# Performance work log

Measured on AMD Instinct MI355X. Metric: run time of the kernel, lower is better.

## Reference

```python
import jax, jax.numpy as jnp
import numpy as np
from jax import lax

# ---- constants matching init_kwargs ----
NY, NX = 1024, 1024
DX, DY = 50.0, 50.0
TTOT = 32.0
DTMAX = 0.5
RHO, G, FD = 910.0, 9.81, 1e-17
EPS = 1e-10
T_FREQ = 5.0
N_STEPS = 64            # fixed step count (>= TTOT/DTMAX); dt masked to 0 once time >= TTOT
LAPSE = 0.0065          # degC per m elevation lapse rate (SMB model)
MELT_FACTOR = 0.5       # m ice / (degC * yr) ablation factor (SMB model)


def update_smb(Z_surf, precip, T_ma_lowest, T_mj_lowest, ice_mask):
    # Lapse-rate temperatures at the surface
    T_ma = T_ma_lowest - LAPSE * Z_surf   # mean annual temperature
    T_mj = T_mj_lowest - LAPSE * Z_surf   # mean July temperature
    accumulation = precip * (T_ma < 0.0).astype(Z_surf.dtype)
    ablation = MELT_FACTOR * jnp.maximum(T_mj, 0.0)
    return (accumulation - ablation) * ice_mask


def setup_inputs() -> dict:
    key = jax.random.key(0)
    k1, k2, k3 = jax.random.split(key, 3)
    # smooth mountain topography: 2500 m gaussian massif + small noise
    y = np.arange(NY, dtype=np.float32) * DY
    x = np.arange(NX, dtype=np.float32) * DX
    yy, xx = np.meshgrid(y, x, indexing="ij")
    cy, cx = y.mean(), x.mean()
    sigma = 0.25 * NX * DX
    z = 2500.0 * np.exp(-((yy - cy) ** 2 + (xx - cx) ** 2) / (2.0 * sigma ** 2))
    Z_topo = jnp.asarray(z, dtype=jnp.float32) + 5.0 * jax.random.normal(k1, (NY, NX), dtype=jnp.float32)
    precip_tensor = 2.0 * jax.random.uniform(k2, (NY, NX), dtype=jnp.float32)  # m ice / yr
    T_ma_lowest = jnp.float32(8.0) + jax.random.normal(k3, (), dtype=jnp.float32)
    T_mj_lowest = T_ma_lowest + jnp.float32(8.0)
    ice_mask = jnp.ones((NY, NX), dtype=jnp.float32)
    return {"precip_tensor": precip_tensor, "T_ma_lowest": T_ma_lowest,
            "T_mj_lowest": T_mj_lowest, "Z_topo": Z_topo, "ice_mask": ice_mask}


def _glacier_step(carry, _, Z_topo, precip, T_ma_lowest, T_mj_lowest, ice_mask):
    H_ice, Z_surf, smb, time, t_last = carry
    # staggered-grid averages and slopes (SIA diffusion)
    H_avg = 0.25 * (H_ice[:-1, :-1] + H_ice[1:, 1:] + H_ice[:-1, 1:] + H_ice[1:, :-1])
    Sx = (Z_surf[:, 1:] - Z_surf[:, :-1]) / DX
    Sy = (Z_surf[1:, :] - Z_surf[:-1, :]) / DY
    Sx = 0.5 * (Sx[:-1, :] + Sx[1:, :])          # (NY-1, NX-1)
    Sy = 0.5 * (Sy[:, :-1] + Sy[:, 1:])          # (NY-1, NX-1)
    Snorm = jnp.sqrt(Sx ** 2 + Sy ** 2 + EPS)
    D = FD * (RHO * G) ** 3 * H_avg ** 5 * Snorm ** 2 + EPS
    # adaptive CFL dt; torch uses .item() so dt is a non-differentiable constant
    dt = jnp.minimum(min(DX, DY) ** 2 / (2.7 * jnp.max(D)), DTMAX)
    dt = lax.stop_gradient(dt)
    dt = jnp.where(time < TTOT, dt, 0.0)         # freeze once ttot is reached
    qx = -(0.5 * (D[:-1, :] + D[1:, :])) * (Z_surf[1:-1, 1:] - Z_surf[1:-1, :-1]) / DX
    qy = -(0.5 * (D[:, :-1] + D[:, 1:])) * (Z_surf[1:, 1:-1] - Z_surf[:-1, 1:-1]) / DY
    dHdt = -(jnp.diff(qx, axis=1) / DX + jnp.diff(qy, axis=0) / DY)  # (NY-2, NX-2)
    H_new = H_ice.at[1:-1, 1:-1].add(dt * (dHdt + smb[1:-1, 1:-1]))
    H_new = jnp.maximum(H_new, 0.0)
    Z_new = Z_topo + H_new
    time = time + dt
    # refresh SMB every T_FREQ model years
    do_upd = (time - t_last) >= T_FREQ
    smb_new = update_smb(Z_new, precip, T_ma_lowest, T_mj_lowest, ice_mask)
    smb = jnp.where(do_upd, smb_new, smb)
    t_last = jnp.where(do_upd, time, t_last)
    return (H_new, Z_new, smb, time, t_last), None


def reference(precip_tensor, T_ma_lowest, T_mj_lowest, Z_topo, ice_mask):
    H_ice = jnp.zeros((NY, NX), dtype=jnp.float32)
    Z_surf = Z_topo + H_ice
    smb = update_smb(Z_surf, precip_tensor, T_ma_lowest, T_mj_lowest, ice_mask)
    time = jnp.float32(0.0)
    t_last = jnp.float32(0.0)
    step = lambda c, x: _glacier_step(c, x, Z_topo, precip_tensor, T_ma_lowest, T_mj_lowest, ice_mask)
    (H_ice, _, _, _, _), _ = lax.scan(step, (H_ice, Z_surf, smb, time, t_last), None, length=N_STEPS)
    return H_ice
```

## Files before the change

kernel.cpp:

```cpp
#include <hip/hip_runtime.h>
#include <math.h>

#define NYg 1024
#define NXg 1024
#define W   1024
#define NSTEPS 64
#define GRID_N (NYg * W)
#define NB    256

#define NSLOT 16
#define SLOT_STRIDE 32
#define SLOT_GROUP  (NSLOT * SLOT_STRIDE)
#define NSLOTG      (NSTEPS + 1)
#define WS_CNT  (NSLOTG * SLOT_GROUP)
#define WS_NBF  (WS_CNT + NSLOT * 32)
#define WS_CTRL_END (WS_NBF + NB * 32)
#define WS_GRIDS 65536

constexpr float DXf   = 50.0f;
constexpr float DYf   = 50.0f;
constexpr float TTOTf = 32.0f;
constexpr float DTMAXf= 0.5f;
constexpr float EPSf  = 1e-10f;
constexpr float TFREQ = 5.0f;
constexpr float LAPSE = 0.0065f;
constexpr float MELTF = 0.5f;
constexpr double RHOG = 910.0 * 9.81;
constexpr float  CDf  = (float)(1e-17 * RHOG * RHOG * RHOG);

__device__ __forceinline__ float scloadf(const float* p) {
    return __hip_atomic_load(p, __ATOMIC_RELAXED, __HIP_MEMORY_SCOPE_SYSTEM);
}
__device__ __forceinline__ void scstoref(float* p, float v) {
    __hip_atomic_store(p, v, __ATOMIC_RELAXED, __HIP_MEMORY_SCOPE_SYSTEM);
}
__device__ __forceinline__ unsigned scloadu(const unsigned* p) {
    return __hip_atomic_load(p, __ATOMIC_RELAXED, __HIP_MEMORY_SCOPE_SYSTEM);
}

__device__ __forceinline__ void poll_backoff(int& sp) {
    if (sp < 32) { __builtin_amdgcn_s_sleep(1); ++sp; }
    else           __builtin_amdgcn_s_sleep(8);
}

__device__ __forceinline__ float dfunc(float h00, float h01, float h10, float h11,
                                       float z00, float z01, float z10, float z11)
{
    float havg = 0.25f * (h00 + h11 + h01 + h10);
    float sx = ((z01 - z00) + (z11 - z10)) * (0.5f / DXf);
    float sy = ((z10 - z00) + (z11 - z01)) * (0.5f / DYf);
    float sn = sqrtf(sx * sx + sy * sy + EPSf);
    float h2 = havg * havg;
    float h4 = h2 * h2;
    return CDf * (h4 * havg) * (sn * sn) + EPSf;
}

__global__ __launch_bounds__(256) void k_init(unsigned* __restrict__ ctrl)
{
    int idx = blockIdx.x * blockDim.x + threadIdx.x;
    int stride = gridDim.x * blockDim.x;
    for (int i = idx; i < WS_CTRL_END; i += stride) {
        unsigned v = 0u;
        if (i < SLOT_GROUP && (i & (SLOT_STRIDE - 1)) == 0) v = __float_as_uint(EPSf);
        ctrl[i] = v;
    }
}

__global__ __launch_bounds__(1024, 1) void k_run(
    float* __restrict__ EZ0, float* __restrict__ EZ1,
    float* __restrict__ ED0, float* __restrict__ ED1,
    const float* __restrict__ ztopo, const float* __restrict__ precip,
    const float* __restrict__ mask, const float* __restrict__ tma,
    const float* __restrict__ tmj, unsigned* __restrict__ ctrl,
    float* __restrict__ Hout)
{
    __shared__ float sZ[7][W];
    __shared__ float sHm[5][W];
    __shared__ float sD[6][W];
    __shared__ unsigned su[NSLOT];
    __shared__ float smax16[16];

    unsigned* slots = ctrl;
    unsigned* cnt   = ctrl + WS_CNT;
    unsigned* nbf   = ctrl + WS_NBF;

    const int c   = threadIdx.x;
    const int b   = blockIdx.x;
    const int r0  = b * 4;
    const int grp = b & (NSLOT - 1);
    const int lane = c & 63, wid = c >> 6;
    const bool hasA = (b > 0), hasB = (b < NB - 1);

    const float TMA = tma[0], TMJ = tmj[0];

    float smbr[5], ztr[5], hN[5], zN[5];
    float dh[5], hOld[5], zOld[5];
    bool inter[5];

    auto c1row = [&](int rr) {
        int r = r0 + rr;
        float zc = 0.0f, hc = 0.0f, d = 0.0f;
        bool iv = false;
        if (r < NYg) {
            zc = sZ[rr + 1][c];
            hc = sHm[rr][c];
            iv = (r >= 1 && r <= NYg - 2 && c >= 1 && c <= NXg - 2);
            if (iv) {
                float zl = sZ[rr + 1][c - 1], zr = sZ[rr + 1][c + 1];
                float zt = sZ[rr][c],         zb = sZ[rr + 2][c];
                float d00 = sD[rr][c - 1],     d01 = sD[rr][c];
                float d10 = sD[rr + 1][c - 1], d11 = sD[rr + 1][c];
                float qxR = -0.5f * (d01 + d11) * (zr - zc) * (1.0f / DXf);
                float qxL = -0.5f * (d00 + d10) * (zc - zl) * (1.0f / DXf);
                float qyB = -0.5f * (d10 + d11) * (zb - zc) * (1.0f / DYf);
                float qyT = -0.5f * (d00 + d01) * (zc - zt) * (1.0f / DYf);
                d = -((qxR - qxL) * (1.0f / DXf) + (qyB - qyT) * (1.0f / DYf));
            }
        }
        dh[rr] = d; hOld[rr] = hc; zOld[rr] = zc; inter[rr] = iv;
    };

    #pragma unroll
    for (int q = 0; q < 7; ++q) {
        int r = r0 - 1 + q;
        sZ[q][c] = (r >= 0 && r < NYg) ? ztopo[r * W + c] : 0.0f;
    }
    #pragma unroll
    for (int q = 0; q < 5; ++q) sHm[q][c] = 0.0f;
    #pragma unroll
    for (int q = 0; q < 6; ++q) sD[q][c] = EPSf;
    #pragma unroll
    for (int rr = 0; rr < 5; ++rr) {
        int r = r0 + rr;
        if (r < NYg) {
            float z = ztopo[r * W + c];
            ztr[rr] = z;
            float t_ma = TMA - LAPSE * z;
            float t_mj = TMJ - LAPSE * z;
            float acc  = (t_ma < 0.0f) ? precip[r * W + c] : 0.0f;
            float abl  = MELTF * fmaxf(t_mj, 0.0f);
            smbr[rr] = (acc - abl) * mask[r * W + c];
        } else { ztr[rr] = 0.0f; smbr[rr] = 0.0f; }
    }
    __syncthreads();

    float t = 0.0f, tl = 0.0f;

    for (int s = 0; s < NSTEPS; ++s) {
        const float* EZr = (s & 1) ? EZ1 : EZ0;
        float*       EZw = (s & 1) ? EZ0 : EZ1;
        const float* EDr = (s & 1) ? ED1 : ED0;
        float*       EDw = (s & 1) ? ED0 : ED1;

        if (s > 0) {
            if (c == 0 && hasA) {
                int sp = 0;
                while (scloadu(&nbf[(b - 1) * 32]) < (unsigned)s) poll_backoff(sp);
            }
            if (c == 64 && hasB) {
                int sp = 0;
                while (scloadu(&nbf[(b + 1) * 32]) < (unsigned)s) poll_backoff(sp);
            }
            __syncthreads();
            float zA = 0.0f, zB = 0.0f, dA = 0.0f, dB = 0.0f;
            if (hasA) { zA = scloadf(EZr + (r0 - 1) * W + c);
                        if (c <= NXg - 2) dA = scloadf(EDr + (r0 - 1) * W + c); }
            if (hasB) { zB = scloadf(EZr + (r0 + 5) * W + c);
                        if (c <= NXg - 2) dB = scloadf(EDr + (r0 + 4) * W + c); }
            c1row(1); c1row(2); c1row(3);
            if (hasA) { sZ[0][c] = zA; if (c <= NXg - 2) sD[0][c] = dA; }
            if (hasB) { sZ[6][c] = zB; if (c <= NXg - 2) sD[5][c] = dB; }
            __syncthreads();
            c1row(0); c1row(4);
        } else {
            c1row(0); c1row(1); c1row(2); c1row(3); c1row(4);
        }

        if (c < NSLOT) {
            unsigned tgt = 16u * (unsigned)s;
            int sp = 0;
            while (scloadu(&cnt[c * 32]) < tgt) poll_backoff(sp);
            su[c] = scloadu(&slots[s * SLOT_GROUP + c * SLOT_STRIDE]);
        }
        __syncthreads();

        unsigned mb = su[0];
        #pragma unroll
        for (int q = 1; q < NSLOT; ++q) mb = max(mb, su[q]);
        float mD = __uint_as_float(mb);
        float dt = fminf(2500.0f / (2.7f * mD), DTMAXf);
        if (!(t < TTOTf)) dt = 0.0f;
        float nt  = t + dt;
        bool  upd = (nt - tl) >= TFREQ;

        #pragma unroll
        for (int rr = 0; rr < 5; ++rr) {
            int r = r0 + rr;
            float h, z;
            if (r >= NYg)        { h = 0.0f; z = 0.0f; }
            else if (inter[rr])  { h = fmaxf(hOld[rr] + dt * (dh[rr] + smbr[rr]), 0.0f);
                                   z = ztr[rr] + h; }
            else                 { h = 0.0f; z = zOld[rr]; }
            hN[rr] = h; zN[rr] = z;
            if (r < NYg) { sZ[rr + 1][c] = z; sHm[rr][c] = h; }
        }
        __syncthreads();

        if (s < NSTEPS - 1) {
            float m = 0.0f, d0 = 0.0f, d3 = 0.0f;
            #pragma unroll
            for (int rr = 0; rr < 4; ++rr) {
                int i = r0 + rr;
                if (i <= NYg - 2 && c <= NXg - 2) {
                    float d = dfunc(sHm[rr][c], sHm[rr][c + 1],
                                    sHm[rr + 1][c], sHm[rr + 1][c + 1],
                                    sZ[rr + 1][c], sZ[rr + 1][c + 1],
                                    sZ[rr + 2][c], sZ[rr + 2][c + 1]);
                    sD[rr + 1][c] = d;
                    m = fmaxf(m, d);
                    if (rr == 0) d0 = d;
                    if (rr == 3) d3 = d;
                }
            }
            #pragma unroll
            for (int off = 32; off >= 1; off >>= 1)
                m = fmaxf(m, __shfl_xor(m, off, 64));
            if (lane == 0) smax16[wid] = m;
            __syncthreads();
            if (c == 0) {
                #pragma unroll
                for (int q = 1; q < 16; ++q) m = fmaxf(m, smax16[q]);
                __hip_atomic_fetch_max(&slots[(s + 1) * SLOT_GROUP + grp * SLOT_STRIDE],
                                       __float_as_uint(m),
                                       __ATOMIC_RELAXED, __HIP_MEMORY_SCOPE_SYSTEM);
                asm volatile("s_waitcnt vmcnt(0)" ::: "memory");
                __hip_atomic_fetch_add(&cnt[grp * 32], 1u,
                                       __ATOMIC_RELAXED, __HIP_MEMORY_SCOPE_SYSTEM);
            }
            if (hasA) {
                scstoref(EZw + (r0 + 1) * W + c, zN[1]);
                if (c <= NXg - 2 && r0 <= NYg - 2) scstoref(EDw + r0 * W + c, d0);
            }
            if (hasB) {
                scstoref(EZw + (r0 + 3) * W + c, zN[3]);
                if (c <= NXg - 2 && r0 + 3 <= NYg - 2) scstoref(EDw + (r0 + 3) * W + c, d3);
            }
            asm volatile("s_waitcnt vmcnt(0)" ::: "memory");
            __syncthreads();
            if (c == 0)
                __hip_atomic_store(&nbf[b * 32], (unsigned)(s + 1),
                                   __ATOMIC_RELAXED, __HIP_MEMORY_SCOPE_SYSTEM);

            if (upd) {
                #pragma unroll
                for (int rr = 0; rr < 5; ++rr) {
                    int r = r0 + rr;
                    if (r < NYg) {
                        float z = zN[rr];
                        float t_ma = TMA - LAPSE * z;
                        float t_mj = TMJ - LAPSE * z;
                        float acc  = (t_ma < 0.0f) ? precip[r * W + c] : 0.0f;
                        float abl  = MELTF * fmaxf(t_mj, 0.0f);
                        smbr[rr] = (acc - abl) * mask[r * W + c];
                    }
                }
            }
        }

        t = nt;
        if (upd) tl = nt;
    }

    #pragma unroll
    for (int rr = 0; rr < 4; ++rr)
        Hout[(r0 + rr) * W + c] = hN[rr];
}

extern "C" void kernel_launch(void* const* d_in, const int* in_sizes, int n_in,
                              void* d_out, int out_size, void* d_ws, size_t ws_size,
                              hipStream_t stream)
{
    const float* precip = (const float*)d_in[0];
    const float* tma    = (const float*)d_in[1];
    const float* tmj    = (const float*)d_in[2];
    const float* ztopo  = (const float*)d_in[3];
    const float* mask   = (const float*)d_in[4];

    unsigned* ctrl = (unsigned*)d_ws;
    float* g = (float*)d_ws + WS_GRIDS;
    float* EZ0 = g + 0 * GRID_N;
    float* EZ1 = g + 1 * GRID_N;
    float* ED0 = g + 2 * GRID_N;
    float* ED1 = g + 3 * GRID_N;

    k_init<<<dim3(64), dim3(256), 0, stream>>>(ctrl);

    k_run<<<dim3(NB), dim3(1024), 0, stream>>>(EZ0, EZ1, ED0, ED1,
                                               ztopo, precip, mask, tma, tmj,
                                               ctrl, (float*)d_out);
}
```

Baseline: 466.0 us.

## Replace counter-based global barrier with per-block max slots polled in parallel

Each block now writes its local max diffusivity into its own slot per step (nonzero value doubles as a ready flag), and 256 threads poll all slots in parallel and reduce with shuffles. This replaces the atomic fetch-max and fetch-add counters and the separate neighbor flags. The dt is computed before the flux pass, so the update is fused into the row computation and one barrier and round trip per step are removed. Halo readiness is implied by the slot write that follows the halo stores. Risk: 256 pollers per block add memory traffic, and correctness relies on the slot store being ordered after the halo stores (vmcnt wait plus barrier).

After: 587.9 us. +26.2%, slower.

```diff
diff --git a/kernel.cpp b/kernel.cpp
--- a/kernel.cpp
+++ b/kernel.cpp
@@ -8,13 +8,8 @@
 #define GRID_N (NYg * W)
 #define NB    256
 
-#define NSLOT 16
-#define SLOT_STRIDE 32
-#define SLOT_GROUP  (NSLOT * SLOT_STRIDE)
-#define NSLOTG      (NSTEPS + 1)
-#define WS_CNT  (NSLOTG * SLOT_GROUP)
-#define WS_NBF  (WS_CNT + NSLOT * 32)
-#define WS_CTRL_END (WS_NBF + NB * 32)
+#define NSLOTG (NSTEPS + 1)
+#define WS_CTRL_END (NSLOTG * NB)
 #define WS_GRIDS 65536
 
 constexpr float DXf   = 50.0f;
@@ -37,6 +32,9 @@
 __device__ __forceinline__ unsigned scloadu(const unsigned* p) {
     return __hip_atomic_load(p, __ATOMIC_RELAXED, __HIP_MEMORY_SCOPE_SYSTEM);
 }
+__device__ __forceinline__ void scstoreu(unsigned* p, unsigned v) {
+    __hip_atomic_store(p, v, __ATOMIC_RELAXED, __HIP_MEMORY_SCOPE_SYSTEM);
+}
 
 __device__ __forceinline__ void poll_backoff(int& sp) {
     if (sp < 32) { __builtin_amdgcn_s_sleep(1); ++sp; }
@@ -59,11 +57,8 @@
 {
     int idx = blockIdx.x * blockDim.x + threadIdx.x;
     int stride = gridDim.x * blockDim.x;
-    for (int i = idx; i < WS_CTRL_END; i += stride) {
-        unsigned v = 0u;
-        if (i < SLOT_GROUP && (i & (SLOT_STRIDE - 1)) == 0) v = __float_as_uint(EPSf);
-        ctrl[i] = v;
-    }
+    for (int i = idx; i < WS_CTRL_END; i += stride) ctrl[i] = 0u;
+    if (idx < NB) ctrl[idx] = __float_as_uint(EPSf);
 }
 
 __global__ __launch_bounds__(1024, 1) void k_run(
@@ -71,41 +66,32 @@
     float* __restrict__ ED0, float* __restrict__ ED1,
     const float* __restrict__ ztopo, const float* __restrict__ precip,
     const float* __restrict__ mask, const float* __restrict__ tma,
-    const float* __restrict__ tmj, unsigned* __restrict__ ctrl,
+    const float* __restrict__ tmj, unsigned* __restrict__ slots,
     float* __restrict__ Hout)
 {
     __shared__ float sZ[7][W];
     __shared__ float sHm[5][W];
     __shared__ float sD[6][W];
-    __shared__ unsigned su[NSLOT];
+    __shared__ unsigned su4[4];
     __shared__ float smax16[16];
-
-    unsigned* slots = ctrl;
-    unsigned* cnt   = ctrl + WS_CNT;
-    unsigned* nbf   = ctrl + WS_NBF;
 
     const int c   = threadIdx.x;
     const int b   = blockIdx.x;
     const int r0  = b * 4;
-    const int grp = b & (NSLOT - 1);
     const int lane = c & 63, wid = c >> 6;
     const bool hasA = (b > 0), hasB = (b < NB - 1);
 
     const float TMA = tma[0], TMJ = tmj[0];
 
     float smbr[5], ztr[5], hN[5], zN[5];
-    float dh[5], hOld[5], zOld[5];
-    bool inter[5];
-
-    auto c1row = [&](int rr) {
+    float dtS = 0.0f;
+
+    auto crow = [&](int rr) {
         int r = r0 + rr;
-        float zc = 0.0f, hc = 0.0f, d = 0.0f;
-        bool iv = false;
+        float h, z;
         if (r < NYg) {
-            zc = sZ[rr + 1][c];
-            hc = sHm[rr][c];
-            iv = (r >= 1 && r <= NYg - 2 && c >= 1 && c <= NXg - 2);
-            if (iv) {
+            float zc = sZ[rr + 1][c];
+            if (r >= 1 && r <= NYg - 2 && c >= 1 && c <= NXg - 2) {
                 float zl = sZ[rr + 1][c - 1], zr = sZ[rr + 1][c + 1];
                 float zt = sZ[rr][c],         zb = sZ[rr + 2][c];
                 float d00 = sD[rr][c - 1],     d01 = sD[rr][c];
@@ -114,10 +100,12 @@
                 float qxL = -0.5f * (d00 + d10) * (zc - zl) * (1.0f / DXf);
                 float qyB = -0.5f * (d10 + d11) * (zb - zc) * (1.0f / DYf);
                 float qyT = -0.5f * (d00 + d01) * (zc - zt) * (1.0f / DYf);
-                d = -((qxR - qxL) * (1.0f / DXf) + (qyB - qyT) * (1.0f / DYf));
-            }
-        }
-        dh[rr] = d; hOld[rr] = hc; zOld[rr] = zc; inter[rr] = iv;
+                float dHdt = -((qxR - qxL) * (1.0f / DXf) + (qyB - qyT) * (1.0f / DYf));
+                h = fmaxf(sHm[rr][c] + dtS * (dHdt + smbr[rr]), 0.0f);
+                z = ztr[rr] + h;
+            } else { h = 0.0f; z = zc; }
+        } else { h = 0.0f; z = 0.0f; }
+        hN[rr] = h; zN[rr] = z;
     };
 
     #pragma unroll
@@ -152,57 +140,44 @@
         const float* EDr = (s & 1) ? ED1 : ED0;
         float*       EDw = (s & 1) ? ED0 : ED1;
 
+        unsigned um = 0u;
+        if (c < NB) {
+            const unsigned* sp_ = &slots[s * NB + c];
+            int sp = 0;
+            while ((um = scloadu(sp_)) == 0u) poll_backoff(sp);
+        }
+        #pragma unroll
+        for (int off = 32; off >= 1; off >>= 1)
+            um = max(um, (unsigned)__shfl_xor((int)um, off, 64));
+        if (c < NB && lane == 0) su4[wid] = um;
+        __syncthreads();
+        unsigned mb = max(max(su4[0], su4[1]), max(su4[2], su4[3]));
+        float mD = __uint_as_float(mb);
+        dtS = fminf(2500.0f / (2.7f * mD), DTMAXf);
+        if (!(t < TTOTf)) dtS = 0.0f;
+        float nt  = t + dtS;
+        bool  upd = (nt - tl) >= TFREQ;
+
         if (s > 0) {
-            if (c == 0 && hasA) {
-                int sp = 0;
-                while (scloadu(&nbf[(b - 1) * 32]) < (unsigned)s) poll_backoff(sp);
-            }
-            if (c == 64 && hasB) {
-                int sp = 0;
-                while (scloadu(&nbf[(b + 1) * 32]) < (unsigned)s) poll_backoff(sp);
-            }
-            __syncthreads();
             float zA = 0.0f, zB = 0.0f, dA = 0.0f, dB = 0.0f;
             if (hasA) { zA = scloadf(EZr + (r0 - 1) * W + c);
                         if (c <= NXg - 2) dA = scloadf(EDr + (r0 - 1) * W + c); }
             if (hasB) { zB = scloadf(EZr + (r0 + 5) * W + c);
                         if (c <= NXg - 2) dB = scloadf(EDr + (r0 + 4) * W + c); }
-            c1row(1); c1row(2); c1row(3);
+            crow(1); crow(2); crow(3);
             if (hasA) { sZ[0][c] = zA; if (c <= NXg - 2) sD[0][c] = dA; }
             if (hasB) { sZ[6][c] = zB; if (c <= NXg - 2) sD[5][c] = dB; }
             __syncthreads();
-            c1row(0); c1row(4);
+            crow(0); crow(4);
         } else {
-            c1row(0); c1row(1); c1row(2); c1row(3); c1row(4);
-        }
-
-        if (c < NSLOT) {
-            unsigned tgt = 16u * (unsigned)s;
-            int sp = 0;
-            while (scloadu(&cnt[c * 32]) < tgt) poll_backoff(sp);
-            su[c] = scloadu(&slots[s * SLOT_GROUP + c * SLOT_STRIDE]);
+            crow(0); crow(1); crow(2); crow(3); crow(4);
         }
         __syncthreads();
-
-        unsigned mb = su[0];
-        #pragma unroll
-        for (int q = 1; q < NSLOT; ++q) mb = max(mb, su[q]);
-        float mD = __uint_as_float(mb);
-        float dt = fminf(2500.0f / (2.7f * mD), DTMAXf);
-        if (!(t < TTOTf)) dt = 0.0f;
-        float nt  = t + dt;
-        bool  upd = (nt - tl) >= TFREQ;
 
         #pragma unroll
         for (int rr = 0; rr < 5; ++rr) {
             int r = r0 + rr;
-            float h, z;
-            if (r >= NYg)        { h = 0.0f; z = 0.0f; }
-            else if (inter[rr])  { h = fmaxf(hOld[rr] + dt * (dh[rr] + smbr[rr]), 0.0f);
-                                   z = ztr[rr] + h; }
-            else                 { h = 0.0f; z = zOld[rr]; }
-            hN[rr] = h; zN[rr] = z;
-            if (r < NYg) { sZ[rr + 1][c] = z; sHm[rr][c] = h; }
+            if (r < NYg) { sZ[rr + 1][c] = zN[rr]; sHm[rr][c] = hN[rr]; }
         }
         __syncthreads();
 
@@ -222,35 +197,25 @@
                     if (rr == 3) d3 = d;
                 }
             }
+            if (hasA) {
+                scstoref(EZw + (r0 + 1) * W + c, zN[1]);
+                if (c <= NXg - 2) scstoref(EDw + r0 * W + c, d0);
+            }
+            if (hasB) {
+                scstoref(EZw + (r0 + 3) * W + c, zN[3]);
+                if (c <= NXg - 2) scstoref(EDw + (r0 + 3) * W + c, d3);
+            }
             #pragma unroll
             for (int off = 32; off >= 1; off >>= 1)
                 m = fmaxf(m, __shfl_xor(m, off, 64));
             if (lane == 0) smax16[wid] = m;
+            asm volatile("s_waitcnt vmcnt(0)" ::: "memory");
             __syncthreads();
             if (c == 0) {
                 #pragma unroll
                 for (int q = 1; q < 16; ++q) m = fmaxf(m, smax16[q]);
-                __hip_atomic_fetch_max(&slots[(s + 1) * SLOT_GROUP + grp * SLOT_STRIDE],
-                                       __float_as_uint(m),
-                                       __ATOMIC_RELAXED, __HIP_MEMORY_SCOPE_SYSTEM);
-                asm volatile("s_waitcnt vmcnt(0)" ::: "memory");
-                __hip_atomic_fetch_add(&cnt[grp * 32], 1u,
-                                       __ATOMIC_RELAXED, __HIP_MEMORY_SCOPE_SYSTEM);
-            }
-            if (hasA) {
-                scstoref(EZw + (r0 + 1) * W + c, zN[1]);
-                if (c <= NXg - 2 && r0 <= NYg - 2) scstoref(EDw + r0 * W + c, d0);
-            }
-            if (hasB) {
-                scstoref(EZw + (r0 + 3) * W + c, zN[3]);
-                if (c <= NXg - 2 && r0 + 3 <= NYg - 2) scstoref(EDw + (r0 + 3) * W + c, d3);
-            }
-            asm volatile("s_waitcnt vmcnt(0)" ::: "memory");
-            __syncthreads();
-            if (c == 0)
-                __hip_atomic_store(&nbf[b * 32], (unsigned)(s + 1),
-                                   __ATOMIC_RELAXED, __HIP_MEMORY_SCOPE_SYSTEM);
-
+                scstoreu(&slots[(s + 1) * NB + b], __float_as_uint(m));
+            }
             if (upd) {
                 #pragma unroll
                 for (int rr = 0; rr < 5; ++rr) {
```
